# Performance work log

Measured on AMD Instinct MI355X. Metric: run time of the kernel, lower is better.

The kernel has to match this reference:

```python
import jax, jax.numpy as jnp
import numpy as np
from jax import lax

# retina / model config (matches init_kwargs)
G, K, S = 64, 3, 2            # first patch size, n scales, scale factor
B, C, H, W = 64, 3, 512, 512  # input batch
C1, C2 = 64, 128              # feature extractor channels


def setup_inputs() -> dict:
    key = jax.random.key(0)
    k1, k2, k3, k4 = jax.random.split(key, 4)
    x = jax.random.normal(k1, (B, C, H, W), jnp.float32)
    # normalized fixation coords in [-1, 1]
    l = jax.random.uniform(k2, (B, 2), jnp.float32, minval=-1.0, maxval=1.0)
    w1 = jax.random.normal(k3, (C1, C, 3, 3), jnp.float32) * 0.05
    b1 = jnp.zeros((C1,), jnp.float32)
    w2 = jax.random.normal(k4, (C2, C1, 3, 3), jnp.float32) * 0.05
    b2 = jnp.zeros((C2,), jnp.float32)
    return {"x": x, "l": l, "w1": w1, "b1": b1, "w2": w2, "b2": b2}


def _conv(x, w, stride):
    return lax.conv_general_dilated(
        x, w, (stride, stride), 'SAME',
        dimension_numbers=('NCHW', 'OIHW', 'NCHW'))


def _extract_patches(x, coords, size):
    """Batched equivalent of crude_retina.extract_patch.

    Torch pads by size//2+1 only when the crop exceeds the image; padding
    unconditionally and offsetting the start indices yields identical values.
    x: (B,C,H,W), coords: (B,2) int [y,x]. Returns (B,C,size,size).
    """
    pad = size // 2 + 1
    xp = jnp.pad(x, ((0, 0), (0, 0), (pad, pad), (pad, pad)))
    start_y = coords[:, 0] - size // 2 + pad
    start_x = coords[:, 1] - size // 2 + pad

    def slice_one(im, sy, sx):
        return lax.dynamic_slice(im, (0, sy, sx), (im.shape[0], size, size))

    return jax.vmap(slice_one)(xp, start_y, start_x)


def _resize_nearest(p, g):
    # torch F.interpolate(mode='nearest'): src = floor(dst * in/out)
    size = p.shape[-1]
    idx = (jnp.arange(g) * size) // g
    return p[:, :, idx][:, :, :, idx]


def reference(x, l, w1, b1, w2, b2):
    T = jnp.array([H, W], jnp.float32)
    # to_exocentric: floor(0.5*(l+1)*T) clamped to [0, max(H,W)]
    coords = jnp.clip(jnp.floor(0.5 * (l + 1.0) * T), 0, max(H, W)).astype(jnp.int32)

    # multi-scale foveation
    phi = []
    size = G
    for _ in range(K):
        p = _extract_patches(x, coords, size)
        if size != G:
            p = _resize_nearest(p, G)
        phi.append(p)
        size = int(S * size)
    phi = jnp.stack(phi, axis=1)  # (B, K, C, G, G)

    # feature extractor applied per patch scale
    outs = []
    for i in range(K):
        h = jax.nn.relu(_conv(phi[:, i], w1, 1) + b1[:, None, None])
        h = jax.nn.relu(_conv(h, w2, 2) + b2[:, None, None])
        outs.append(h)
    return jnp.stack(outs, axis=1)  # (B, K, C2, G//2, G//2)
```

## Files before the change

kernel.cpp:

```cpp
#include <hip/hip_runtime.h>
#include <hip/hip_bf16.h>

typedef __attribute__((ext_vector_type(4))) float  f32x4;
typedef __attribute__((ext_vector_type(8))) _Float16 f16x8;

#define LDA1 40

static __device__ __forceinline__ void gld_lds16(const void* g, void* l) {
    __builtin_amdgcn_global_load_lds(
        (const __attribute__((address_space(1))) void*)g,
        (__attribute__((address_space(3))) void*)l, 16, 0, 0);
}

__global__ void transform_kernel(const float* __restrict__ w1, const float* __restrict__ w2,
                                 _Float16* __restrict__ Bt1, _Float16* __restrict__ Bt2)
{
    const int i = blockIdx.x * 256 + threadIdx.x;
    if (i < 64 * 32) {
        const int n = i >> 5, k = i & 31;
        const float v = (k < 27) ? w1[n * 27 + k] : 0.0f;
        Bt1[i] = (_Float16)v;
    }
    const int j = i - 64 * 32;
    if (j >= 0 && j < 9 * 128 * 64) {
        const int tap = j / (128 * 64);
        const int rem = j % (128 * 64);
        const int n = rem >> 6;
        const int c1 = rem & 63;
        Bt2[j] = (_Float16)w2[((size_t)n * 64 + c1) * 9 + tap];
    }
}

__global__ __launch_bounds__(256) void conv1_mfma(
    const float* __restrict__ x, const float* __restrict__ l,
    const _Float16* __restrict__ Bt1, const float* __restrict__ b1,
    _Float16* __restrict__ h1, int bk0)
{
    const int img = blockIdx.y;
    const int bk  = bk0 + img;
    const int b   = bk / 3, ksc = bk % 3;
    const int step = 1 << ksc;
    const int half = 32 << ksc;
    const int mbase = blockIdx.x * 256;

    const float ly = l[b * 2 + 0], lx = l[b * 2 + 1];
    int cy = (int)floorf(0.5f * (ly + 1.0f) * 512.0f);
    int cx = (int)floorf(0.5f * (lx + 1.0f) * 512.0f);
    cy = min(max(cy, 0), 512);
    cx = min(max(cx, 0), 512);
    const int sy = cy - half, sx = cx - half;

    __shared__ _Float16 A_lds[256 * LDA1];

    const int t = threadIdx.x;
    {
        const int m  = mbase + t;
        const int py = m >> 6, px = m & 63;
        const float* xb = x + (size_t)b * 3 * 512 * 512;
        _Float16* arow = &A_lds[t * LDA1];
        #pragma unroll
        for (int k = 0; k < 27; ++k) {
            const int c = k / 9, r = k % 9, kh = r / 3, kw = r % 3;
            const int yy = py + kh - 1, xx = px + kw - 1;
            const int iy = sy + yy * step, ix = sx + xx * step;
            float v = 0.0f;
            if (yy >= 0 && yy < 64 && xx >= 0 && xx < 64 &&
                iy >= 0 && iy < 512 && ix >= 0 && ix < 512)
                v = xb[(size_t)c * 512 * 512 + iy * 512 + ix];
            arow[k] = (_Float16)v;
        }
        #pragma unroll
        for (int k = 27; k < 32; ++k) arow[k] = (_Float16)0.0f;
    }
    __syncthreads();

    const int wave = t >> 6, lane = t & 63;
    const int lrow = lane & 15, kb = lane >> 4;

    f16x8 bfr[4];
    #pragma unroll
    for (int nf = 0; nf < 4; ++nf)
        bfr[nf] = *(const f16x8*)(Bt1 + ((size_t)(nf * 16 + lrow)) * 32 + kb * 8);

    f32x4 acc[4][4];
    #pragma unroll
    for (int mf = 0; mf < 4; ++mf)
        #pragma unroll
        for (int nf = 0; nf < 4; ++nf)
            #pragma unroll
            for (int r = 0; r < 4; ++r) acc[mf][nf][r] = 0.0f;

    #pragma unroll
    for (int mf = 0; mf < 4; ++mf) {
        const int mrow = wave * 4 + mf;
        const f16x8 afr = *(const f16x8*)(&A_lds[(mrow * 16 + lrow) * LDA1 + kb * 8]);
        #pragma unroll
        for (int nf = 0; nf < 4; ++nf)
            acc[mf][nf] = __builtin_amdgcn_mfma_f32_16x16x32_f16(afr, bfr[nf], acc[mf][nf], 0, 0, 0);
    }

    _Float16* hb = h1 + (size_t)img * 4096 * 64;
    #pragma unroll
    for (int mf = 0; mf < 4; ++mf) {
        const int m0 = mbase + (wave * 4 + mf) * 16 + kb * 4;
        #pragma unroll
        for (int nf = 0; nf < 4; ++nf) {
            const int c1 = nf * 16 + lrow;
            const float bb = b1[c1];
            #pragma unroll
            for (int r = 0; r < 4; ++r) {
                const float v = fmaxf(acc[mf][nf][r] + bb, 0.0f);
                const int mm = m0 + r;
                const int ps = (mm & ~63) | ((mm & 1) << 5) | ((mm & 63) >> 1);
                const int c1s = c1 ^ ((ps & 7) << 3);
                hb[(size_t)ps * 64 + c1s] = (_Float16)v;
            }
        }
    }
}

__global__ __launch_bounds__(256) void conv2_mfma(
    const _Float16* __restrict__ h1, const _Float16* __restrict__ Bt2,
    const float* __restrict__ b2, float* __restrict__ out, int bk0)
{
    const int img = blockIdx.y;
    const int bk  = bk0 + img;
    const int mc  = blockIdx.x;
    const int t = threadIdx.x, wave = t >> 6, lane = t & 63;
    const int lrow = lane & 15, kb = lane >> 4;

    __shared__ _Float16 As[5 * 4096 + 2 * 8192];
    _Float16* Bs = As + 5 * 4096;

    const _Float16* hb = h1 + (size_t)img * 4096 * 64;
    const int ys = mc * 4;
    const int nrows = (mc == 15) ? 4 : 5;

    if (mc == 15) {
        f16x8 z = {};
        *(f16x8*)&As[4 * 4096 + t * 16]     = z;
        *(f16x8*)&As[4 * 4096 + t * 16 + 8] = z;
    }

    {
        const _Float16* ga = hb + (size_t)ys * 4096;
        #pragma unroll
        for (int j = 0; j < 10; ++j) {
            if (j < nrows * 2) {
                const int c = j * 256 + t;
                gld_lds16(ga + (size_t)c * 8, As + (j * 256 + wave * 64) * 8);
            }
        }
    }
    {
        #pragma unroll
        for (int i = 0; i < 4; ++i) {
            const int c = i * 256 + t;
            const int r = c >> 3, j = c & 7;
            const int jt = j ^ (r & 7);
            gld_lds16(Bt2 + (size_t)r * 64 + jt * 8,
                      Bs + (i * 256 + wave * 64) * 8);
        }
    }

    f32x4 acc[8];
    #pragma unroll
    for (int nf = 0; nf < 8; ++nf)
        #pragma unroll
        for (int r = 0; r < 4; ++r) acc[nf][r] = 0.0f;

    const int mloc = wave * 16 + lrow;
    const int q  = mloc >> 5;
    const int ox = mloc & 31;

    #pragma unroll 1
    for (int tap = 0; tap < 9; ++tap) {
        __syncthreads();
        if (tap < 8) {
            const _Float16* gb = Bt2 + (size_t)(tap + 1) * 8192;
            const int slot = (tap + 1) & 1;
            #pragma unroll
            for (int i = 0; i < 4; ++i) {
                const int c = i * 256 + t;
                const int r = c >> 3, j = c & 7;
                const int jt = j ^ (r & 7);
                gld_lds16(gb + (size_t)r * 64 + jt * 8,
                          Bs + slot * 8192 + (i * 256 + wave * 64) * 8);
            }
        }
        const int kh = tap / 3, kw = tap % 3;
        const int rrow = 2 * q + kh;
        const int par  = kw & 1;
        const int xh   = ox + (kw >> 1);
        const int p    = rrow * 64 + par * 32 + xh;
        const bool kill = (kw == 2) && (ox == 31);
        const int slot = tap & 1;

        #pragma unroll
        for (int c1h = 0; c1h < 2; ++c1h) {
            const int jt = c1h * 4 + kb;
            f16x8 afr = *(const f16x8*)&As[p * 64 + (jt ^ (p & 7)) * 8];
            if (kill) afr = (f16x8){};
            #pragma unroll
            for (int nf = 0; nf < 8; ++nf) {
                const int r = nf * 16 + lrow;
                const f16x8 bfr = *(const f16x8*)&Bs[slot * 8192 + r * 64 + (jt ^ (r & 7)) * 8];
                acc[nf] = __builtin_amdgcn_mfma_f32_16x16x32_f16(afr, bfr, acc[nf], 0, 0, 0);
            }
        }
    }

    float* ob = out + (size_t)bk * 128 * 1024;
    const int m0 = mc * 64 + wave * 16 + kb * 4;
    #pragma unroll
    for (int nf = 0; nf < 8; ++nf) {
        const int c2 = nf * 16 + lrow;
        const float bb = b2[c2];
        f32x4 v;
        #pragma unroll
        for (int r = 0; r < 4; ++r) v[r] = fmaxf(acc[nf][r] + bb, 0.0f);
        *(f32x4*)(ob + (size_t)c2 * 1024 + m0) = v;
    }
}

extern "C" void kernel_launch(void* const* d_in, const int* in_sizes, int n_in,
                              void* d_out, int out_size, void* d_ws, size_t ws_size,
                              hipStream_t stream) {
    const float* x  = (const float*)d_in[0];
    const float* l  = (const float*)d_in[1];
    const float* w1 = (const float*)d_in[2];
    const float* b1 = (const float*)d_in[3];
    const float* w2 = (const float*)d_in[4];
    const float* b2 = (const float*)d_in[5];
    float* out = (float*)d_out;

    _Float16* Bt1 = (_Float16*)d_ws;
    _Float16* Bt2 = Bt1 + 64 * 32;
    _Float16* h1  = (_Float16*)((char*)d_ws + 160 * 1024);

    const int total_imgs = 192;
    const size_t per_img = (size_t)4096 * 64 * sizeof(_Float16);
    size_t h1_cap = (ws_size > 160 * 1024) ? ws_size - 160 * 1024 : 0;
    int ipc = (int)(h1_cap / per_img);
    if (ipc > total_imgs) ipc = total_imgs;
    if (ipc < 1) ipc = 1;

    transform_kernel<<<296, 256, 0, stream>>>(w1, w2, Bt1, Bt2);

    for (int bk0 = 0; bk0 < total_imgs; bk0 += ipc) {
        const int n = (total_imgs - bk0 < ipc) ? (total_imgs - bk0) : ipc;
        conv1_mfma<<<dim3(16, n), 256, 0, stream>>>(x, l, Bt1, b1, h1, bk0);
        conv2_mfma<<<dim3(16, n), 256, 0, stream>>>(h1, Bt2, b2, out, bk0);
    }
}
```

Measured before the change: 115.7 us.

## Stage input patch in LDS, coalesce h1 stores, retile conv2 waves 2x4

After: 102.6 us (median of 3 runs). 11.3% less time.

```diff
diff --git a/kernel.cpp b/kernel.cpp
--- a/kernel.cpp
+++ b/kernel.cpp
@@ -41,7 +41,7 @@
     const int b   = bk / 3, ksc = bk % 3;
     const int step = 1 << ksc;
     const int half = 32 << ksc;
-    const int mbase = blockIdx.x * 256;
+    const int py0 = blockIdx.x * 4;
 
     const float ly = l[b * 2 + 0], lx = l[b * 2 + 1];
     int cy = (int)floorf(0.5f * (ly + 1.0f) * 512.0f);
@@ -50,24 +50,33 @@
     cx = min(max(cx, 0), 512);
     const int sy = cy - half, sx = cx - half;
 
+    __shared__ float    patch[3 * 6 * 66];
     __shared__ _Float16 A_lds[256 * LDA1];
+    __shared__ _Float16 out_t[256 * 64];
 
     const int t = threadIdx.x;
+    const float* xb = x + (size_t)b * 3 * 512 * 512;
+    for (int i = t; i < 3 * 6 * 66; i += 256) {
+        const int c  = i / 396, r = i % 396;
+        const int ry = r / 66, xx = r % 66;
+        const int yy = py0 - 1 + ry;
+        const int col = xx - 1;
+        const int iy = sy + yy * step, ix = sx + col * step;
+        float v = 0.0f;
+        if (yy >= 0 && yy < 64 && col >= 0 && col < 64 &&
+            iy >= 0 && iy < 512 && ix >= 0 && ix < 512)
+            v = xb[(size_t)c * 262144 + iy * 512 + ix];
+        patch[i] = v;
+    }
+    __syncthreads();
+
     {
-        const int m  = mbase + t;
-        const int py = m >> 6, px = m & 63;
-        const float* xb = x + (size_t)b * 3 * 512 * 512;
+        const int pyl = t >> 6, px = t & 63;
         _Float16* arow = &A_lds[t * LDA1];
         #pragma unroll
         for (int k = 0; k < 27; ++k) {
-            const int c = k / 9, r = k % 9, kh = r / 3, kw = r % 3;
-            const int yy = py + kh - 1, xx = px + kw - 1;
-            const int iy = sy + yy * step, ix = sx + xx * step;
-            float v = 0.0f;
-            if (yy >= 0 && yy < 64 && xx >= 0 && xx < 64 &&
-                iy >= 0 && iy < 512 && ix >= 0 && ix < 512)
-                v = xb[(size_t)c * 512 * 512 + iy * 512 + ix];
-            arow[k] = (_Float16)v;
+            const int c = k / 9, rr = k % 9, kh = rr / 3, kw = rr % 3;
+            arow[k] = (_Float16)patch[c * 396 + (pyl + kh) * 66 + (px + kw)];
         }
         #pragma unroll
         for (int k = 27; k < 32; ++k) arow[k] = (_Float16)0.0f;
@@ -92,17 +101,15 @@
 
     #pragma unroll
     for (int mf = 0; mf < 4; ++mf) {
-        const int mrow = wave * 4 + mf;
-        const f16x8 afr = *(const f16x8*)(&A_lds[(mrow * 16 + lrow) * LDA1 + kb * 8]);
+        const f16x8 afr = *(const f16x8*)(&A_lds[((wave * 4 + mf) * 16 + lrow) * LDA1 + kb * 8]);
         #pragma unroll
         for (int nf = 0; nf < 4; ++nf)
             acc[mf][nf] = __builtin_amdgcn_mfma_f32_16x16x32_f16(afr, bfr[nf], acc[mf][nf], 0, 0, 0);
     }
 
-    _Float16* hb = h1 + (size_t)img * 4096 * 64;
     #pragma unroll
     for (int mf = 0; mf < 4; ++mf) {
-        const int m0 = mbase + (wave * 4 + mf) * 16 + kb * 4;
+        const int ml0 = (wave * 4 + mf) * 16 + kb * 4;
         #pragma unroll
         for (int nf = 0; nf < 4; ++nf) {
             const int c1 = nf * 16 + lrow;
@@ -110,12 +117,22 @@
             #pragma unroll
             for (int r = 0; r < 4; ++r) {
                 const float v = fmaxf(acc[mf][nf][r] + bb, 0.0f);
-                const int mm = m0 + r;
-                const int ps = (mm & ~63) | ((mm & 1) << 5) | ((mm & 63) >> 1);
-                const int c1s = c1 ^ ((ps & 7) << 3);
-                hb[(size_t)ps * 64 + c1s] = (_Float16)v;
-            }
-        }
+                const int ml = ml0 + r;
+                const int xcol = ml & 63;
+                const int psx = ((xcol & 1) << 5) | (xcol >> 1);
+                const int pl  = (ml & ~63) | psx;
+                const int c1s = c1 ^ ((psx & 7) << 3);
+                out_t[pl * 64 + c1s] = (_Float16)v;
+            }
+        }
+    }
+    __syncthreads();
+
+    _Float16* hb = h1 + (size_t)img * 4096 * 64 + (size_t)py0 * 64 * 64;
+    #pragma unroll
+    for (int j = 0; j < 8; ++j) {
+        const int idx = j * 256 + t;
+        *(f16x8*)(hb + (size_t)idx * 8) = *(const f16x8*)&out_t[idx * 8];
     }
 }
 
@@ -128,6 +145,8 @@
     const int mc  = blockIdx.x;
     const int t = threadIdx.x, wave = t >> 6, lane = t & 63;
     const int lrow = lane & 15, kb = lane >> 4;
+    const int wq = wave >> 1;
+    const int wn = wave & 1;
 
     __shared__ _Float16 As[5 * 4096 + 2 * 8192];
     _Float16* Bs = As + 5 * 4096;
@@ -163,15 +182,13 @@
         }
     }
 
-    f32x4 acc[8];
-    #pragma unroll
-    for (int nf = 0; nf < 8; ++nf)
-        #pragma unroll
-        for (int r = 0; r < 4; ++r) acc[nf][r] = 0.0f;
-
-    const int mloc = wave * 16 + lrow;
-    const int q  = mloc >> 5;
-    const int ox = mloc & 31;
+    f32x4 acc[2][4];
+    #pragma unroll
+    for (int mf = 0; mf < 2; ++mf)
+        #pragma unroll
+        for (int nf = 0; nf < 4; ++nf)
+            #pragma unroll
+            for (int r = 0; r < 4; ++r) acc[mf][nf][r] = 0.0f;
 
     #pragma unroll 1
     for (int tap = 0; tap < 9; ++tap) {
@@ -189,37 +206,47 @@
             }
         }
         const int kh = tap / 3, kw = tap % 3;
-        const int rrow = 2 * q + kh;
-        const int par  = kw & 1;
-        const int xh   = ox + (kw >> 1);
-        const int p    = rrow * 64 + par * 32 + xh;
-        const bool kill = (kw == 2) && (ox == 31);
+        const int par = kw & 1;
+        const int rrow = 2 * wq + kh;
         const int slot = tap & 1;
 
         #pragma unroll
         for (int c1h = 0; c1h < 2; ++c1h) {
             const int jt = c1h * 4 + kb;
-            f16x8 afr = *(const f16x8*)&As[p * 64 + (jt ^ (p & 7)) * 8];
-            if (kill) afr = (f16x8){};
-            #pragma unroll
-            for (int nf = 0; nf < 8; ++nf) {
-                const int r = nf * 16 + lrow;
+            f16x8 afr[2];
+            #pragma unroll
+            for (int mf = 0; mf < 2; ++mf) {
+                const int ox = mf * 16 + lrow;
+                const int xh = ox + (kw >> 1);
+                const int p  = rrow * 64 + par * 32 + xh;
+                f16x8 v = *(const f16x8*)&As[p * 64 + (jt ^ (p & 7)) * 8];
+                if ((kw == 2) && (ox == 31)) v = (f16x8){};
+                afr[mf] = v;
+            }
+            #pragma unroll
+            for (int nf = 0; nf < 4; ++nf) {
+                const int r = wn * 64 + nf * 16 + lrow;
                 const f16x8 bfr = *(const f16x8*)&Bs[slot * 8192 + r * 64 + (jt ^ (r & 7)) * 8];
-                acc[nf] = __builtin_amdgcn_mfma_f32_16x16x32_f16(afr, bfr, acc[nf], 0, 0, 0);
+                #pragma unroll
+                for (int mf = 0; mf < 2; ++mf)
+                    acc[mf][nf] = __builtin_amdgcn_mfma_f32_16x16x32_f16(afr[mf], bfr, acc[mf][nf], 0, 0, 0);
             }
         }
     }
 
     float* ob = out + (size_t)bk * 128 * 1024;
-    const int m0 = mc * 64 + wave * 16 + kb * 4;
-    #pragma unroll
-    for (int nf = 0; nf < 8; ++nf) {
-        const int c2 = nf * 16 + lrow;
-        const float bb = b2[c2];
-        f32x4 v;
-        #pragma unroll
-        for (int r = 0; r < 4; ++r) v[r] = fmaxf(acc[nf][r] + bb, 0.0f);
-        *(f32x4*)(ob + (size_t)c2 * 1024 + m0) = v;
+    #pragma unroll
+    for (int mf = 0; mf < 2; ++mf) {
+        const int m0 = mc * 64 + wq * 32 + mf * 16 + kb * 4;
+        #pragma unroll
+        for (int nf = 0; nf < 4; ++nf) {
+            const int c2 = wn * 64 + nf * 16 + lrow;
+            const float bb = b2[c2];
+            f32x4 v;
+            #pragma unroll
+            for (int r = 0; r < 4; ++r) v[r] = fmaxf(acc[mf][nf][r] + bb, 0.0f);
+            *(f32x4*)(ob + (size_t)c2 * 1024 + m0) = v;
+        }
     }
 }
 
```
